# Performance work log

Measured on AMD Instinct MI355X. Metric: run time of the kernel, lower is better.

## Reference

```python
import jax, jax.numpy as jnp
import numpy as np
from jax import lax

W_WIN = 7  # window size from init_kwargs


def _dwconv(x, k):
    """Depthwise 2D conv, SAME padding, kernel k: [C,1,kh,kw] (OIHW)."""
    C = x.shape[1]
    p = k.shape[-1] // 2
    return lax.conv_general_dilated(
        x, k, window_strides=(1, 1), padding=[(p, p), (p, p)],
        feature_group_count=C, dimension_numbers=("NCHW", "OIHW", "NCHW"))


def setup_inputs() -> dict:
    key = jax.random.key(0)
    ks = jax.random.split(key, 6)
    B, C, H, Wd = 1, 48, 56, 56
    x = jax.random.normal(ks[0], (B, C, H, Wd), dtype=jnp.float32)
    # small init scale keeps the softmax logits (dot/49) in a sane range
    w3 = jax.random.normal(ks[1], (C, 1, 3, 3), dtype=jnp.float32) * 0.1
    w5 = jax.random.normal(ks[2], (C, 1, 5, 5), dtype=jnp.float32) * 0.1
    w7 = jax.random.normal(ks[3], (C, 1, 7, 7), dtype=jnp.float32) * 0.1
    pw = jax.random.normal(ks[4], (C, 3 * C, 1, 1), dtype=jnp.float32) * 0.05
    pb = jax.random.normal(ks[5], (C,), dtype=jnp.float32) * 0.01
    return {"x": x, "w3": w3, "w5": w5, "w7": w7, "pw": pw, "pb": pb}


def reference(x, w3, w5, w7, pw, pb):
    B, C, H, Wd = x.shape
    w = W_WIN
    # multi-scale depthwise branch, concat on channels -> [B, 3C, H, W]
    y = jnp.concatenate([_dwconv(x, w3), _dwconv(x, w5), _dwconv(x, w7)], axis=1)
    pad_h = (-H) % w
    pad_w = (-Wd) % w
    if pad_h or pad_w:  # static Python ints -> jit-safe
        y = jnp.pad(y, ((0, 0), (0, 0), (0, pad_h), (0, pad_w)), mode="reflect")
    Hp, Wp = y.shape[2], y.shape[3]
    nH, nW = Hp // w, Wp // w
    C3 = 3 * C
    # equivalent to torch unfold(2,w,w).unfold(3,w,w).permute(0,1,2,4,3,5)
    # .reshape(B,3C,nH*nW,w*w): same row-major linearization
    yw = y.reshape(B, C3, nH * nW, w * w)
    # rows: (B, nH*nW, 3C) flattened -> N x (w*w)
    yf = yw.transpose(0, 2, 1, 3).reshape(B * nH * nW * C3, w * w)
    # full N x N self-attention over all rows (faithful to the original)
    attn = jax.nn.softmax((yf @ yf.T) / (w * w), axis=-1)
    y_hat = (attn @ yf).reshape(B, nH, nW, C3, w, w)
    y_hat = y_hat.transpose(0, 3, 1, 4, 2, 5).reshape(B, C3, nH * w, nW * w)
    y_hat = y_hat[:, :, :H, :Wd]
    # 1x1 projection 3C -> C, plus residual
    out = jnp.einsum("oi,bihw->bohw", pw[:, :, 0, 0], y_hat) + pb[None, :, None, None]
    return x + out
```

## Files before the change

### kernel.cpp

```cpp
#include <hip/hip_runtime.h>

typedef unsigned int uint;
typedef unsigned short ushort;
typedef __attribute__((ext_vector_type(8))) short bf16x8;
typedef __attribute__((ext_vector_type(4))) float f32x4;

#define C_IN   48
#define C3     144
#define HW     56
#define SSP    3136
#define DW     49
#define DPAD   64
#define NROWS  9216

#define NSPLIT 8
#define TPS    18

#define CSC 0.02944245f

#define YF_B    0
#define YFT_B   1179648
#define OPART_B 2359296
#define ESUM_B  (OPART_B + NSPLIT * DW * NROWS * 2)

__device__ __forceinline__ ushort f32_to_bf16_rne(float x) {
  uint b = __float_as_uint(x);
  b += 0x7fffu + ((b >> 16) & 1u);
  return (ushort)(b >> 16);
}
__device__ __forceinline__ float bf16_to_f32(ushort u) {
  return __uint_as_float(((uint)u) << 16);
}
__device__ __forceinline__ void async_copy16(const void* g, void* l) {
  __builtin_amdgcn_global_load_lds(
      (const __attribute__((address_space(1))) unsigned int*)g,
      (__attribute__((address_space(3))) unsigned int*)l, 16, 0, 0);
}

__global__ __launch_bounds__(256) void conv_kernel(
    const float* __restrict__ x, const float* __restrict__ w3,
    const float* __restrict__ w5, const float* __restrict__ w7,
    ushort* __restrict__ yf, ushort* __restrict__ yfT) {
  int idx = blockIdx.x * 256 + threadIdx.x;
  int r = idx >> 6, t = idx & 63;
  if (t >= DW) {
    yf[idx] = 0;
    if (t == 56) yfT[56 * NROWS + r] = 0x3F80;
    return;
  }
  int g = r / C3, c3 = r - g * C3;
  int flat = g * DW + t;
  int h = flat / HW, w = flat - h * HW;
  int grp = c3 / C_IN, c = c3 - grp * C_IN;
  const float* wk; int ks;
  if (grp == 0)      { wk = w3 + c * 9;  ks = 3; }
  else if (grp == 1) { wk = w5 + c * 25; ks = 5; }
  else               { wk = w7 + c * 49; ks = 7; }
  int p = ks >> 1;
  const float* xc = x + c * SSP;
  float val = 0.f;
  for (int dy = 0; dy < ks; dy++) {
    int hy = h + dy - p;
    if (hy < 0 || hy >= HW) continue;
    const float* xr = xc + hy * HW;
    const float* wr = wk + dy * ks;
    for (int dx = 0; dx < ks; dx++) {
      int wx = w + dx - p;
      if (wx < 0 || wx >= HW) continue;
      val += xr[wx] * wr[dx];
    }
  }
  ushort ov = f32_to_bf16_rne(val);
  yf[idx] = ov;
  yfT[t * NROWS + r] = ov;
}

__global__ __launch_bounds__(256, 3) void attn_kernel(
    const ushort* __restrict__ yf, const ushort* __restrict__ yfT,
    ushort* __restrict__ opart, float* __restrict__ esum_g) {
  __shared__ __align__(16) char smem[51200];

  const int tid = threadIdx.x;
  const int w = tid >> 6, lane = tid & 63;
  const int q = lane >> 4, c = lane & 15;
  const int m0 = blockIdx.x * 128 + w * 32;
  const int sp = blockIdx.y;
  ushort* Pm = (ushort*)(smem + 32768) + w * (32 * 72);

  bf16x8 qf[2][2];
#pragma unroll
  for (int mt = 0; mt < 2; mt++)
#pragma unroll
    for (int ds = 0; ds < 2; ds++) {
      bf16x8 raw = *(const bf16x8*)&yf[(m0 + mt * 16 + c) * 64 + ds * 32 + q * 8];
      short tmp[8];
#pragma unroll
      for (int j = 0; j < 8; j++)
        tmp[j] = (short)f32_to_bf16_rne(bf16_to_f32((ushort)raw[j]) * CSC);
      qf[mt][ds] = *(bf16x8*)tmp;
    }

  f32x4 o[4][2];
#pragma unroll
  for (int dt = 0; dt < 4; dt++)
#pragma unroll
    for (int mt = 0; mt < 2; mt++) o[dt][mt] = (f32x4)0.f;

  const int s0 = w, s1 = w + 4;

  {
    const int k0 = (sp * TPS) * 64;
    char* Kb = smem;
    char* Vb = smem + 16384;
    async_copy16(yf + (k0 + lane) * 64 + s0 * 8, Kb + s0 * 1024);
    async_copy16(yf + (k0 + lane) * 64 + s1 * 8, Kb + s1 * 1024);
    async_copy16(yfT + lane * NROWS + k0 + s0 * 8, Vb + s0 * 1024);
    async_copy16(yfT + lane * NROWS + k0 + s1 * 8, Vb + s1 * 1024);
  }
  __syncthreads();

  for (int it = 0; it < TPS; it++) {
    const int cur = it & 1;
    if (it + 1 < TPS) {
      const int k1 = (sp * TPS + it + 1) * 64;
      char* Kb = smem + (cur ^ 1) * 8192;
      char* Vb = smem + 16384 + (cur ^ 1) * 8192;
      async_copy16(yf + (k1 + lane) * 64 + s0 * 8, Kb + s0 * 1024);
      async_copy16(yf + (k1 + lane) * 64 + s1 * 8, Kb + s1 * 1024);
      async_copy16(yfT + lane * NROWS + k1 + s0 * 8, Vb + s0 * 1024);
      async_copy16(yfT + lane * NROWS + k1 + s1 * 8, Vb + s1 * 1024);
    }

    const char* Kb = smem + cur * 8192;
    const char* Vb = smem + 16384 + cur * 8192;

    f32x4 s[4][2];
#pragma unroll
    for (int nt = 0; nt < 4; nt++) {
      bf16x8 a0 = *(const bf16x8*)(Kb + q * 1024 + (nt * 16 + c) * 16);
      bf16x8 a1 = *(const bf16x8*)(Kb + (4 + q) * 1024 + (nt * 16 + c) * 16);
      s[nt][0] = (f32x4)0.f; s[nt][1] = (f32x4)0.f;
      s[nt][0] = __builtin_amdgcn_mfma_f32_16x16x32_bf16(a0, qf[0][0], s[nt][0], 0, 0, 0);
      s[nt][1] = __builtin_amdgcn_mfma_f32_16x16x32_bf16(a0, qf[1][0], s[nt][1], 0, 0, 0);
      s[nt][0] = __builtin_amdgcn_mfma_f32_16x16x32_bf16(a1, qf[0][1], s[nt][0], 0, 0, 0);
      s[nt][1] = __builtin_amdgcn_mfma_f32_16x16x32_bf16(a1, qf[1][1], s[nt][1], 0, 0, 0);
    }

#pragma unroll
    for (int nt = 0; nt < 4; nt++)
#pragma unroll
      for (int mt = 0; mt < 2; mt++) {
        f32x4 sv = s[nt][mt];
        float p0 = __builtin_amdgcn_exp2f(sv[0]);
        float p1 = __builtin_amdgcn_exp2f(sv[1]);
        float p2 = __builtin_amdgcn_exp2f(sv[2]);
        float p3 = __builtin_amdgcn_exp2f(sv[3]);
        uint d0 = (__float_as_uint(p0) >> 16) | (__float_as_uint(p1) & 0xffff0000u);
        uint d1 = (__float_as_uint(p2) >> 16) | (__float_as_uint(p3) & 0xffff0000u);
        *(uint2*)&Pm[(mt * 16 + c) * 72 + nt * 16 + q * 4] = make_uint2(d0, d1);
      }

    bf16x8 bp[2][2];
#pragma unroll
    for (int mt = 0; mt < 2; mt++)
#pragma unroll
      for (int nc = 0; nc < 2; nc++)
        bp[mt][nc] = *(const bf16x8*)&Pm[(mt * 16 + c) * 72 + nc * 32 + q * 8];
#pragma unroll
    for (int dt = 0; dt < 4; dt++) {
      bf16x8 v0 = *(const bf16x8*)(Vb + q * 1024 + (dt * 16 + c) * 16);
      bf16x8 v1 = *(const bf16x8*)(Vb + (4 + q) * 1024 + (dt * 16 + c) * 16);
      o[dt][0] = __builtin_amdgcn_mfma_f32_16x16x32_bf16(v0, bp[0][0], o[dt][0], 0, 0, 0);
      o[dt][1] = __builtin_amdgcn_mfma_f32_16x16x32_bf16(v0, bp[1][0], o[dt][1], 0, 0, 0);
      o[dt][0] = __builtin_amdgcn_mfma_f32_16x16x32_bf16(v1, bp[0][1], o[dt][0], 0, 0, 0);
      o[dt][1] = __builtin_amdgcn_mfma_f32_16x16x32_bf16(v1, bp[1][1], o[dt][1], 0, 0, 0);
    }

    if (it + 1 < TPS) __syncthreads();
  }

#pragma unroll
  for (int dt = 0; dt < 4; dt++)
#pragma unroll
    for (int mt = 0; mt < 2; mt++)
#pragma unroll
      for (int r = 0; r < 4; r++) {
        int d = dt * 16 + q * 4 + r;
        int m = m0 + mt * 16 + c;
        float v = o[dt][mt][r];
        if (d < DW) {
          opart[(sp * DW + d) * NROWS + m] = f32_to_bf16_rne(v);
        } else if (d == 56) {
          esum_g[sp * NROWS + m] = v;
        }
      }
}

__global__ __launch_bounds__(256) void fuse_pw_kernel(
    const ushort* __restrict__ opart, const float* __restrict__ esum_g,
    const float* __restrict__ x, const float* __restrict__ pw,
    const float* __restrict__ pb, float* __restrict__ out) {
  __shared__ float vb[7 * 145];
  __shared__ float inv_es[144];
  const int g = blockIdx.x, tch = blockIdx.y;
  const int t0 = tch * 7;
  const int tid = threadIdx.x;

  if (tid < 144) {
    int r = g * C3 + tid;
    float e = 0.f;
#pragma unroll
    for (int sp = 0; sp < NSPLIT; sp++) e += esum_g[sp * NROWS + r];
    inv_es[tid] = 1.f / e;
  }
  __syncthreads();

  for (int j = tid; j < 7 * 144; j += 256) {
    int tt = j / 144, i = j - tt * 144;
    int r = g * C3 + i, t = t0 + tt;
    float ov = 0.f;
#pragma unroll
    for (int sp = 0; sp < NSPLIT; sp++)
      ov += bf16_to_f32(opart[(sp * DW + t) * NROWS + r]);
    vb[tt * 145 + i] = ov * inv_es[i];
  }
  __syncthreads();

  for (int j = tid; j < C_IN * 7; j += 256) {
    int o = j / 7, tt = j - o * 7;
    int t = t0 + tt;
    const float* pwo = pw + o * C3;
    const float* vrow = &vb[tt * 145];
    float a0 = 0.f, a1 = 0.f, a2 = 0.f, a3 = 0.f;
#pragma unroll
    for (int i = 0; i < C3; i += 4) {
      float4 wv = *(const float4*)&pwo[i];
      a0 += wv.x * vrow[i];
      a1 += wv.y * vrow[i + 1];
      a2 += wv.z * vrow[i + 2];
      a3 += wv.w * vrow[i + 3];
    }
    float acc = (a0 + a1) + (a2 + a3);
    int nh = g >> 3, nw = g & 7;
    int th = t / 7, tw = t - th * 7;
    int oidx = o * SSP + (nh * 7 + th) * HW + (nw * 7 + tw);
    out[oidx] = x[oidx] + pb[o] + acc;
  }
}

extern "C" void kernel_launch(void* const* d_in, const int* in_sizes, int n_in,
                              void* d_out, int out_size, void* d_ws, size_t ws_size,
                              hipStream_t stream) {
  const float* x  = (const float*)d_in[0];
  const float* w3 = (const float*)d_in[1];
  const float* w5 = (const float*)d_in[2];
  const float* w7 = (const float*)d_in[3];
  const float* pw = (const float*)d_in[4];
  const float* pb = (const float*)d_in[5];
  float* out = (float*)d_out;
  char* ws = (char*)d_ws;

  ushort* yf    = (ushort*)(ws + YF_B);
  ushort* yfT   = (ushort*)(ws + YFT_B);
  ushort* opart = (ushort*)(ws + OPART_B);
  float*  esum  = (float*)(ws + ESUM_B);

  conv_kernel<<<(NROWS * DPAD) / 256, 256, 0, stream>>>(x, w3, w5, w7, yf, yfT);
  attn_kernel<<<dim3(NROWS / 128, NSPLIT), 256, 0, stream>>>(yf, yfT, opart, esum);
  fuse_pw_kernel<<<dim3(64, 7), 256, 0, stream>>>(opart, esum, x, pw, pb, out);
}
```

Before: 120.2 us.

## Double per-warp query tile, add coalesced transpose kernel, rebalance key splits

The attention kernel now gives each warp 64 query rows instead of 32, so every K/V tile loaded into LDS is reused across twice as many MFMAs. The grid changes to 36x12 blocks with 12 key tiles per split, and the P stride in shared memory is reduced to 68. The transposed V copy is no longer written with scattered stores from the conv kernel; a separate LDS-tiled transpose kernel produces it with coalesced stores. This costs an extra launch, more registers and LDS per block (occupancy drops to 2 blocks), and more partial outputs for the fuse kernel to reduce.

New measurement: 133.1 us. +10.8%, slower.

```diff
diff --git a/kernel.cpp b/kernel.cpp
--- a/kernel.cpp
+++ b/kernel.cpp
@@ -13,8 +13,8 @@
 #define DPAD   64
 #define NROWS  9216
 
-#define NSPLIT 8
-#define TPS    18
+#define NSPLIT 12
+#define TPS    12
 
 #define CSC 0.02944245f
 
@@ -23,6 +23,8 @@
 #define OPART_B 2359296
 #define ESUM_B  (OPART_B + NSPLIT * DW * NROWS * 2)
 
+#define PSTRIDE 68
+
 __device__ __forceinline__ ushort f32_to_bf16_rne(float x) {
   uint b = __float_as_uint(x);
   b += 0x7fffu + ((b >> 16) & 1u);
@@ -40,14 +42,10 @@
 __global__ __launch_bounds__(256) void conv_kernel(
     const float* __restrict__ x, const float* __restrict__ w3,
     const float* __restrict__ w5, const float* __restrict__ w7,
-    ushort* __restrict__ yf, ushort* __restrict__ yfT) {
+    ushort* __restrict__ yf) {
   int idx = blockIdx.x * 256 + threadIdx.x;
   int r = idx >> 6, t = idx & 63;
-  if (t >= DW) {
-    yf[idx] = 0;
-    if (t == 56) yfT[56 * NROWS + r] = 0x3F80;
-    return;
-  }
+  if (t >= DW) { yf[idx] = 0; return; }
   int g = r / C3, c3 = r - g * C3;
   int flat = g * DW + t;
   int h = flat / HW, w = flat - h * HW;
@@ -70,26 +68,43 @@
       val += xr[wx] * wr[dx];
     }
   }
-  ushort ov = f32_to_bf16_rne(val);
-  yf[idx] = ov;
-  yfT[t * NROWS + r] = ov;
-}
-
-__global__ __launch_bounds__(256, 3) void attn_kernel(
+  yf[idx] = f32_to_bf16_rne(val);
+}
+
+__global__ __launch_bounds__(256) void transpose_kernel(
+    const ushort* __restrict__ yf, ushort* __restrict__ yfT) {
+  __shared__ ushort tile[32][68];
+  const int r0 = blockIdx.x * 32;
+  const int tid = threadIdx.x;
+  const int rr = tid >> 3, cb = (tid & 7) * 8;
+  *(bf16x8*)&tile[rr][cb] = *(const bf16x8*)&yf[(r0 + rr) * 64 + cb];
+  __syncthreads();
+  const int t = tid >> 2, rb = (tid & 3) * 8;
+  ushort tmp[8];
+#pragma unroll
+  for (int i = 0; i < 8; i++) tmp[i] = tile[rb + i][t];
+  if (t == 56) {
+#pragma unroll
+    for (int i = 0; i < 8; i++) tmp[i] = 0x3F80;
+  }
+  *(bf16x8*)&yfT[t * NROWS + r0 + rb] = *(bf16x8*)&tmp[0];
+}
+
+__global__ __launch_bounds__(256, 2) void attn_kernel(
     const ushort* __restrict__ yf, const ushort* __restrict__ yfT,
     ushort* __restrict__ opart, float* __restrict__ esum_g) {
-  __shared__ __align__(16) char smem[51200];
+  __shared__ __align__(16) char smem[67584];
 
   const int tid = threadIdx.x;
   const int w = tid >> 6, lane = tid & 63;
   const int q = lane >> 4, c = lane & 15;
-  const int m0 = blockIdx.x * 128 + w * 32;
+  const int m0 = blockIdx.x * 256 + w * 64;
   const int sp = blockIdx.y;
-  ushort* Pm = (ushort*)(smem + 32768) + w * (32 * 72);
-
-  bf16x8 qf[2][2];
-#pragma unroll
-  for (int mt = 0; mt < 2; mt++)
+  ushort* Pm = (ushort*)(smem + 32768) + w * (64 * PSTRIDE);
+
+  bf16x8 qf[4][2];
+#pragma unroll
+  for (int mt = 0; mt < 4; mt++)
 #pragma unroll
     for (int ds = 0; ds < 2; ds++) {
       bf16x8 raw = *(const bf16x8*)&yf[(m0 + mt * 16 + c) * 64 + ds * 32 + q * 8];
@@ -100,22 +115,20 @@
       qf[mt][ds] = *(bf16x8*)tmp;
     }
 
-  f32x4 o[4][2];
+  f32x4 o[4][4];
 #pragma unroll
   for (int dt = 0; dt < 4; dt++)
 #pragma unroll
-    for (int mt = 0; mt < 2; mt++) o[dt][mt] = (f32x4)0.f;
+    for (int mt = 0; mt < 4; mt++) o[dt][mt] = (f32x4)0.f;
 
   const int s0 = w, s1 = w + 4;
 
   {
     const int k0 = (sp * TPS) * 64;
-    char* Kb = smem;
-    char* Vb = smem + 16384;
-    async_copy16(yf + (k0 + lane) * 64 + s0 * 8, Kb + s0 * 1024);
-    async_copy16(yf + (k0 + lane) * 64 + s1 * 8, Kb + s1 * 1024);
-    async_copy16(yfT + lane * NROWS + k0 + s0 * 8, Vb + s0 * 1024);
-    async_copy16(yfT + lane * NROWS + k0 + s1 * 8, Vb + s1 * 1024);
+    async_copy16(yf + (k0 + lane) * 64 + s0 * 8, smem + s0 * 1024);
+    async_copy16(yf + (k0 + lane) * 64 + s1 * 8, smem + s1 * 1024);
+    async_copy16(yfT + lane * NROWS + k0 + s0 * 8, smem + 16384 + s0 * 1024);
+    async_copy16(yfT + lane * NROWS + k0 + s1 * 8, smem + 16384 + s1 * 1024);
   }
   __syncthreads();
 
@@ -134,46 +147,44 @@
     const char* Kb = smem + cur * 8192;
     const char* Vb = smem + 16384 + cur * 8192;
 
-    f32x4 s[4][2];
 #pragma unroll
     for (int nt = 0; nt < 4; nt++) {
       bf16x8 a0 = *(const bf16x8*)(Kb + q * 1024 + (nt * 16 + c) * 16);
       bf16x8 a1 = *(const bf16x8*)(Kb + (4 + q) * 1024 + (nt * 16 + c) * 16);
-      s[nt][0] = (f32x4)0.f; s[nt][1] = (f32x4)0.f;
-      s[nt][0] = __builtin_amdgcn_mfma_f32_16x16x32_bf16(a0, qf[0][0], s[nt][0], 0, 0, 0);
-      s[nt][1] = __builtin_amdgcn_mfma_f32_16x16x32_bf16(a0, qf[1][0], s[nt][1], 0, 0, 0);
-      s[nt][0] = __builtin_amdgcn_mfma_f32_16x16x32_bf16(a1, qf[0][1], s[nt][0], 0, 0, 0);
-      s[nt][1] = __builtin_amdgcn_mfma_f32_16x16x32_bf16(a1, qf[1][1], s[nt][1], 0, 0, 0);
-    }
-
-#pragma unroll
-    for (int nt = 0; nt < 4; nt++)
-#pragma unroll
-      for (int mt = 0; mt < 2; mt++) {
-        f32x4 sv = s[nt][mt];
-        float p0 = __builtin_amdgcn_exp2f(sv[0]);
-        float p1 = __builtin_amdgcn_exp2f(sv[1]);
-        float p2 = __builtin_amdgcn_exp2f(sv[2]);
-        float p3 = __builtin_amdgcn_exp2f(sv[3]);
+      f32x4 s[4];
+#pragma unroll
+      for (int mt = 0; mt < 4; mt++) {
+        s[mt] = (f32x4)0.f;
+        s[mt] = __builtin_amdgcn_mfma_f32_16x16x32_bf16(a0, qf[mt][0], s[mt], 0, 0, 0);
+        s[mt] = __builtin_amdgcn_mfma_f32_16x16x32_bf16(a1, qf[mt][1], s[mt], 0, 0, 0);
+      }
+#pragma unroll
+      for (int mt = 0; mt < 4; mt++) {
+        float p0 = __builtin_amdgcn_exp2f(s[mt][0]);
+        float p1 = __builtin_amdgcn_exp2f(s[mt][1]);
+        float p2 = __builtin_amdgcn_exp2f(s[mt][2]);
+        float p3 = __builtin_amdgcn_exp2f(s[mt][3]);
         uint d0 = (__float_as_uint(p0) >> 16) | (__float_as_uint(p1) & 0xffff0000u);
         uint d1 = (__float_as_uint(p2) >> 16) | (__float_as_uint(p3) & 0xffff0000u);
-        *(uint2*)&Pm[(mt * 16 + c) * 72 + nt * 16 + q * 4] = make_uint2(d0, d1);
-      }
-
-    bf16x8 bp[2][2];
-#pragma unroll
-    for (int mt = 0; mt < 2; mt++)
+        *(uint2*)&Pm[(mt * 16 + c) * PSTRIDE + nt * 16 + q * 4] = make_uint2(d0, d1);
+      }
+    }
+
+    bf16x8 bp[4][2];
+#pragma unroll
+    for (int mt = 0; mt < 4; mt++)
 #pragma unroll
       for (int nc = 0; nc < 2; nc++)
-        bp[mt][nc] = *(const bf16x8*)&Pm[(mt * 16 + c) * 72 + nc * 32 + q * 8];
+        bp[mt][nc] = *(const bf16x8*)&Pm[(mt * 16 + c) * PSTRIDE + nc * 32 + q * 8];
 #pragma unroll
     for (int dt = 0; dt < 4; dt++) {
       bf16x8 v0 = *(const bf16x8*)(Vb + q * 1024 + (dt * 16 + c) * 16);
       bf16x8 v1 = *(const bf16x8*)(Vb + (4 + q) * 1024 + (dt * 16 + c) * 16);
-      o[dt][0] = __builtin_amdgcn_mfma_f32_16x16x32_bf16(v0, bp[0][0], o[dt][0], 0, 0, 0);
-      o[dt][1] = __builtin_amdgcn_mfma_f32_16x16x32_bf16(v0, bp[1][0], o[dt][1], 0, 0, 0);
-      o[dt][0] = __builtin_amdgcn_mfma_f32_16x16x32_bf16(v1, bp[0][1], o[dt][0], 0, 0, 0);
-      o[dt][1] = __builtin_amdgcn_mfma_f32_16x16x32_bf16(v1, bp[1][1], o[dt][1], 0, 0, 0);
+#pragma unroll
+      for (int mt = 0; mt < 4; mt++) {
+        o[dt][mt] = __builtin_amdgcn_mfma_f32_16x16x32_bf16(v0, bp[mt][0], o[dt][mt], 0, 0, 0);
+        o[dt][mt] = __builtin_amdgcn_mfma_f32_16x16x32_bf16(v1, bp[mt][1], o[dt][mt], 0, 0, 0);
+      }
     }
 
     if (it + 1 < TPS) __syncthreads();
@@ -182,7 +193,7 @@
 #pragma unroll
   for (int dt = 0; dt < 4; dt++)
 #pragma unroll
-    for (int mt = 0; mt < 2; mt++)
+    for (int mt = 0; mt < 4; mt++)
 #pragma unroll
       for (int r = 0; r < 4; r++) {
         int d = dt * 16 + q * 4 + r;
@@ -265,7 +276,8 @@
   ushort* opart = (ushort*)(ws + OPART_B);
   float*  esum  = (float*)(ws + ESUM_B);
 
-  conv_kernel<<<(NROWS * DPAD) / 256, 256, 0, stream>>>(x, w3, w5, w7, yf, yfT);
-  attn_kernel<<<dim3(NROWS / 128, NSPLIT), 256, 0, stream>>>(yf, yfT, opart, esum);
+  conv_kernel<<<(NROWS * DPAD) / 256, 256, 0, stream>>>(x, w3, w5, w7, yf);
+  transpose_kernel<<<NROWS / 32, 256, 0, stream>>>(yf, yfT);
+  attn_kernel<<<dim3(NROWS / 256, NSPLIT), 256, 0, stream>>>(yf, yfT, opart, esum);
   fuse_pw_kernel<<<dim3(64, 7), 256, 0, stream>>>(opart, esum, x, pw, pb, out);
 }
```

## Shuffle attention probabilities via ds_bpermute instead of LDS staging, double key splits

Applied to the files above, without the earlier changes.

The P matrix is no longer written to and read back from shared memory. The exponentiated scores are packed into registers and redistributed into the MFMA B-operand layout with ds_bpermute. This shrinks LDS use from 51200 to 32768 bytes, which lets the launch bound rise to 5 blocks per CU. The key range split also doubles (NSPLIT 16, TPS 9), giving more blocks for parallelism but more partial outputs to reduce. The risks are extra cross-lane traffic, correctness of the permutation mapping, and larger partial-sum writes.

After: 121.5 us. No clear change (+1.1%).

```diff
diff --git a/kernel.cpp b/kernel.cpp
--- a/kernel.cpp
+++ b/kernel.cpp
@@ -13,8 +13,8 @@
 #define DPAD   64
 #define NROWS  9216
 
-#define NSPLIT 8
-#define TPS    18
+#define NSPLIT 16
+#define TPS    9
 
 #define CSC 0.02944245f
 
@@ -75,17 +75,19 @@
   yfT[t * NROWS + r] = ov;
 }
 
-__global__ __launch_bounds__(256, 3) void attn_kernel(
+__global__ __launch_bounds__(256, 5) void attn_kernel(
     const ushort* __restrict__ yf, const ushort* __restrict__ yfT,
     ushort* __restrict__ opart, float* __restrict__ esum_g) {
-  __shared__ __align__(16) char smem[51200];
+  __shared__ __align__(16) char smem[32768];
 
   const int tid = threadIdx.x;
   const int w = tid >> 6, lane = tid & 63;
   const int q = lane >> 4, c = lane & 15;
   const int m0 = blockIdx.x * 128 + w * 32;
   const int sp = blockIdx.y;
-  ushort* Pm = (ushort*)(smem + 32768) + w * (32 * 72);
+
+  const int addrA = ((((q & 1) << 1)) * 16 + c) << 2;
+  const int addrB = addrA + 64;
 
   bf16x8 qf[2][2];
 #pragma unroll
@@ -110,12 +112,10 @@
 
   {
     const int k0 = (sp * TPS) * 64;
-    char* Kb = smem;
-    char* Vb = smem + 16384;
-    async_copy16(yf + (k0 + lane) * 64 + s0 * 8, Kb + s0 * 1024);
-    async_copy16(yf + (k0 + lane) * 64 + s1 * 8, Kb + s1 * 1024);
-    async_copy16(yfT + lane * NROWS + k0 + s0 * 8, Vb + s0 * 1024);
-    async_copy16(yfT + lane * NROWS + k0 + s1 * 8, Vb + s1 * 1024);
+    async_copy16(yf + (k0 + lane) * 64 + s0 * 8, smem + s0 * 1024);
+    async_copy16(yf + (k0 + lane) * 64 + s1 * 8, smem + s1 * 1024);
+    async_copy16(yfT + lane * NROWS + k0 + s0 * 8, smem + 16384 + s0 * 1024);
+    async_copy16(yfT + lane * NROWS + k0 + s1 * 8, smem + 16384 + s1 * 1024);
   }
   __syncthreads();
 
@@ -134,46 +134,48 @@
     const char* Kb = smem + cur * 8192;
     const char* Vb = smem + 16384 + cur * 8192;
 
-    f32x4 s[4][2];
+    uint pk[4][2][2];
 #pragma unroll
     for (int nt = 0; nt < 4; nt++) {
       bf16x8 a0 = *(const bf16x8*)(Kb + q * 1024 + (nt * 16 + c) * 16);
       bf16x8 a1 = *(const bf16x8*)(Kb + (4 + q) * 1024 + (nt * 16 + c) * 16);
-      s[nt][0] = (f32x4)0.f; s[nt][1] = (f32x4)0.f;
-      s[nt][0] = __builtin_amdgcn_mfma_f32_16x16x32_bf16(a0, qf[0][0], s[nt][0], 0, 0, 0);
-      s[nt][1] = __builtin_amdgcn_mfma_f32_16x16x32_bf16(a0, qf[1][0], s[nt][1], 0, 0, 0);
-      s[nt][0] = __builtin_amdgcn_mfma_f32_16x16x32_bf16(a1, qf[0][1], s[nt][0], 0, 0, 0);
-      s[nt][1] = __builtin_amdgcn_mfma_f32_16x16x32_bf16(a1, qf[1][1], s[nt][1], 0, 0, 0);
-    }
-
-#pragma unroll
-    for (int nt = 0; nt < 4; nt++)
+      f32x4 s[2];
+      s[0] = (f32x4)0.f; s[1] = (f32x4)0.f;
+      s[0] = __builtin_amdgcn_mfma_f32_16x16x32_bf16(a0, qf[0][0], s[0], 0, 0, 0);
+      s[1] = __builtin_amdgcn_mfma_f32_16x16x32_bf16(a0, qf[1][0], s[1], 0, 0, 0);
+      s[0] = __builtin_amdgcn_mfma_f32_16x16x32_bf16(a1, qf[0][1], s[0], 0, 0, 0);
+      s[1] = __builtin_amdgcn_mfma_f32_16x16x32_bf16(a1, qf[1][1], s[1], 0, 0, 0);
 #pragma unroll
       for (int mt = 0; mt < 2; mt++) {
-        f32x4 sv = s[nt][mt];
-        float p0 = __builtin_amdgcn_exp2f(sv[0]);
-        float p1 = __builtin_amdgcn_exp2f(sv[1]);
-        float p2 = __builtin_amdgcn_exp2f(sv[2]);
-        float p3 = __builtin_amdgcn_exp2f(sv[3]);
-        uint d0 = (__float_as_uint(p0) >> 16) | (__float_as_uint(p1) & 0xffff0000u);
-        uint d1 = (__float_as_uint(p2) >> 16) | (__float_as_uint(p3) & 0xffff0000u);
-        *(uint2*)&Pm[(mt * 16 + c) * 72 + nt * 16 + q * 4] = make_uint2(d0, d1);
-      }
-
-    bf16x8 bp[2][2];
-#pragma unroll
-    for (int mt = 0; mt < 2; mt++)
-#pragma unroll
-      for (int nc = 0; nc < 2; nc++)
-        bp[mt][nc] = *(const bf16x8*)&Pm[(mt * 16 + c) * 72 + nc * 32 + q * 8];
-#pragma unroll
-    for (int dt = 0; dt < 4; dt++) {
-      bf16x8 v0 = *(const bf16x8*)(Vb + q * 1024 + (dt * 16 + c) * 16);
-      bf16x8 v1 = *(const bf16x8*)(Vb + (4 + q) * 1024 + (dt * 16 + c) * 16);
-      o[dt][0] = __builtin_amdgcn_mfma_f32_16x16x32_bf16(v0, bp[0][0], o[dt][0], 0, 0, 0);
-      o[dt][1] = __builtin_amdgcn_mfma_f32_16x16x32_bf16(v0, bp[1][0], o[dt][1], 0, 0, 0);
-      o[dt][0] = __builtin_amdgcn_mfma_f32_16x16x32_bf16(v1, bp[0][1], o[dt][0], 0, 0, 0);
-      o[dt][1] = __builtin_amdgcn_mfma_f32_16x16x32_bf16(v1, bp[1][1], o[dt][1], 0, 0, 0);
+        float p0 = __builtin_amdgcn_exp2f(s[mt][0]);
+        float p1 = __builtin_amdgcn_exp2f(s[mt][1]);
+        float p2 = __builtin_amdgcn_exp2f(s[mt][2]);
+        float p3 = __builtin_amdgcn_exp2f(s[mt][3]);
+        pk[nt][mt][0] = (__float_as_uint(p0) >> 16) | (__float_as_uint(p1) & 0xffff0000u);
+        pk[nt][mt][1] = (__float_as_uint(p2) >> 16) | (__float_as_uint(p3) & 0xffff0000u);
+      }
+    }
+
+#pragma unroll
+    for (int nc = 0; nc < 2; nc++) {
+      bf16x8 bp[2];
+#pragma unroll
+      for (int mt = 0; mt < 2; mt++) {
+        uint sel0 = (q < 2) ? pk[2 * nc][mt][0] : pk[2 * nc + 1][mt][0];
+        uint sel1 = (q < 2) ? pk[2 * nc][mt][1] : pk[2 * nc + 1][mt][1];
+        uint qa0 = (uint)__builtin_amdgcn_ds_bpermute(addrA, (int)sel0);
+        uint qa1 = (uint)__builtin_amdgcn_ds_bpermute(addrA, (int)sel1);
+        uint qb0 = (uint)__builtin_amdgcn_ds_bpermute(addrB, (int)sel0);
+        uint qb1 = (uint)__builtin_amdgcn_ds_bpermute(addrB, (int)sel1);
+        uint tmp[4] = {qa0, qa1, qb0, qb1};
+        bp[mt] = *(bf16x8*)tmp;
+      }
+#pragma unroll
+      for (int dt = 0; dt < 4; dt++) {
+        bf16x8 va = *(const bf16x8*)(Vb + (nc * 4 + q) * 1024 + (dt * 16 + c) * 16);
+        o[dt][0] = __builtin_amdgcn_mfma_f32_16x16x32_bf16(va, bp[0], o[dt][0], 0, 0, 0);
+        o[dt][1] = __builtin_amdgcn_mfma_f32_16x16x32_bf16(va, bp[1], o[dt][1], 0, 0, 0);
+      }
     }
 
     if (it + 1 < TPS) __syncthreads();
```
